# Kernel tuning notes

Hardware: AMD Instinct MI355X
Metric: run time of the kernel (lower is better)

The kernel has to match this reference:

```python
import jax, jax.numpy as jnp
import numpy as np

B, IN, OUT = 384, 512, 384  # B must equal OUT (broadcast in original sigma_3 + diag(sigma_bias))


def setup_inputs() -> dict:
    key = jax.random.key(0)
    k1, k2, k3, k4 = jax.random.split(key, 4)
    mu = jax.random.normal(k1, (B, IN), dtype=jnp.float32)
    sigma = jax.random.uniform(k2, (B, IN, IN), dtype=jnp.float32)
    # nn.Linear weight: normal(0, 0.1); bias filled with 1e-4
    W = 0.1 * jax.random.normal(k3, (OUT, IN), dtype=jnp.float32)
    b = jnp.full((OUT,), 1e-4, dtype=jnp.float32)
    # sigma_weight ~ U(-12, -2.2); sigma_bias = ones * bias(True)
    sigma_weight = jax.random.uniform(k4, (OUT, IN), minval=-12.0, maxval=-2.2, dtype=jnp.float32)
    sigma_bias = jnp.ones((OUT,), dtype=jnp.float32)
    return {"mu": mu, "sigma": sigma, "W": W, "b": b,
            "sigma_weight": sigma_weight, "sigma_bias": sigma_bias}


def reference(mu, sigma, W, b, sigma_weight, sigma_bias):
    sp = jnp.log1p(jnp.exp(sigma_weight))            # softplus(sigma_weight), [OUT, IN]
    mu_f = mu @ W.T + b                              # [B, OUT]
    # sigma_1: diag( sum_i sigma[b,i,i] * sp[o,i] )  (equivalent to the torch
    # diag_embed / batched-matmul / diagonal chain, without the [B,OUT,IN,IN] blowup)
    diag_sigma = jnp.diagonal(sigma, axis1=1, axis2=2)   # [B, IN]
    s1 = jnp.einsum('bi,oi->bo', diag_sigma, sp)         # [B, OUT]
    # sigma_2 = W @ sigma @ W^T, dense part
    s2 = jnp.einsum('oi,bij,pj->bop', W, sigma, W)       # [B, OUT, OUT]
    # sigma_3 = sp @ mu^2 + diag(sigma_bias)  ([B,OUT] + [OUT,OUT], valid since B==OUT)
    s3 = jnp.square(mu) @ sp.T + jnp.diag(sigma_bias)    # [B, OUT]
    eye = jnp.eye(sp.shape[0], dtype=mu.dtype)
    sigma_out = (s1 + s3)[:, :, None] * eye + s2         # [B, OUT, OUT]
    return mu_f, sigma_out
```

## Files before the change

### kernel.cpp

```cpp
#include <hip/hip_runtime.h>
#include <hip/hip_bf16.h>
#include <math.h>

#define Bn   384
#define INn  512
#define OUTn 384

typedef __bf16 bf16x8 __attribute__((ext_vector_type(8)));
typedef __bf16 bf16x4 __attribute__((ext_vector_type(4)));
typedef float  f32x4  __attribute__((ext_vector_type(4)));

__device__ __bf16 g_Wbf[OUTn * INn];
__device__ float  g_sp [OUTn * INn];
__device__ float  g_d  [Bn * OUTn];
__device__ float  g_t  [Bn * INn];
__device__ __bf16 g_U  [(size_t)Bn * OUTn * INn];

__global__ __launch_bounds__(256) void prep_kernel(const float* __restrict__ W,
                                                   const float* __restrict__ sw) {
    int idx = blockIdx.x * 256 + threadIdx.x;
    if (idx < OUTn * INn) {
        g_Wbf[idx] = (__bf16)W[idx];
        float x = sw[idx];
        g_sp[idx] = (x > 20.f) ? x : log1pf(expf(x));
    }
}

__global__ __launch_bounds__(512, 4) void passA_kernel(const float* __restrict__ sigma) {
    __shared__ __bf16 As[64][INn + 8];

    const int it   = blockIdx.x;
    const int b    = blockIdx.y;
    const int tid  = threadIdx.x;
    const int wave = tid >> 6, lane = tid & 63;
    const int quad = lane >> 4, l15 = lane & 15;
    const int i0   = it * 64;

    const float* sigb = sigma + (size_t)b * (INn * INn) + (size_t)i0 * INn;

#pragma unroll
    for (int k = 0; k < 8; ++k) {
        const int r = k * 8 + wave;
        const float* rp = sigb + (size_t)r * INn + lane * 8;
        float4 a0 = *(const float4*)rp;
        float4 a1 = *(const float4*)(rp + 4);
        bf16x8 t;
        t[0]=(__bf16)a0.x; t[1]=(__bf16)a0.y; t[2]=(__bf16)a0.z; t[3]=(__bf16)a0.w;
        t[4]=(__bf16)a1.x; t[5]=(__bf16)a1.y; t[6]=(__bf16)a1.z; t[7]=(__bf16)a1.w;
        *(bf16x8*)&As[r][lane * 8] = t;
        const int ig = i0 + r;
        if ((ig >> 3) == lane) {
            const int c = ig & 7;
            float dv = (c==0)?a0.x:(c==1)?a0.y:(c==2)?a0.z:(c==3)?a0.w
                     :(c==4)?a1.x:(c==5)?a1.y:(c==6)?a1.z:a1.w;
            g_t[b * INn + ig] = dv;
        }
    }
    __syncthreads();

    const int p_base = wave * 48;
    f32x4 acc[4][3];
#pragma unroll
    for (int mi = 0; mi < 4; ++mi)
#pragma unroll
        for (int nf = 0; nf < 3; ++nf) acc[mi][nf] = (f32x4){0.f, 0.f, 0.f, 0.f};

    for (int kc = 0; kc < INn; kc += 32) {
        bf16x8 afr[4];
#pragma unroll
        for (int mi = 0; mi < 4; ++mi)
            afr[mi] = *(const bf16x8*)&As[mi * 16 + l15][kc + quad * 8];
#pragma unroll
        for (int nf = 0; nf < 3; ++nf) {
            const __bf16* bp = g_Wbf + (size_t)(p_base + nf * 16 + l15) * INn + kc + quad * 8;
            bf16x8 bfr = *(const bf16x8*)bp;
#pragma unroll
            for (int mi = 0; mi < 4; ++mi)
                acc[mi][nf] = __builtin_amdgcn_mfma_f32_16x16x32_bf16(afr[mi], bfr, acc[mi][nf], 0, 0, 0);
        }
    }

    __bf16* Ub = g_U + (size_t)b * (OUTn * INn);
#pragma unroll
    for (int mi = 0; mi < 4; ++mi) {
        const int ib = i0 + mi * 16 + quad * 4;
#pragma unroll
        for (int nf = 0; nf < 3; ++nf) {
            const int p = p_base + nf * 16 + l15;
            bf16x4 v;
            v[0] = (__bf16)acc[mi][nf][0];
            v[1] = (__bf16)acc[mi][nf][1];
            v[2] = (__bf16)acc[mi][nf][2];
            v[3] = (__bf16)acc[mi][nf][3];
            *(bf16x4*)(Ub + (size_t)p * INn + ib) = v;
        }
    }
}

__global__ __launch_bounds__(256) void k2_kernel(const float* __restrict__ mu,
                                                 const float* __restrict__ W,
                                                 const float* __restrict__ bias,
                                                 const float* __restrict__ sbias,
                                                 float* __restrict__ out_muf) {
    const int b  = blockIdx.x;
    const int oq = blockIdx.y;
    __shared__ __align__(16) float muL[INn];
    __shared__ __align__(16) float tL[INn];
    const int tid = threadIdx.x;
    for (int i = tid; i < INn; i += 256) {
        float m = mu[b * INn + i];
        muL[i] = m;
        tL[i] = g_t[b * INn + i] + m * m;
    }
    __syncthreads();
    const int wave = tid >> 6, lane = tid & 63;
    const float4* Mr = (const float4*)muL;
    const float4* Tr = (const float4*)tL;
    float4 m0 = Mr[lane * 2], m1 = Mr[lane * 2 + 1];
    float4 t0 = Tr[lane * 2], t1 = Tr[lane * 2 + 1];
#pragma unroll 4
    for (int ow = 0; ow < 24; ++ow) {
        const int o = oq * 96 + wave * 24 + ow;
        const float4* Wr = (const float4*)(W + (size_t)o * INn);
        const float4* Sr = (const float4*)(g_sp + (size_t)o * INn);
        float4 w0 = Wr[lane * 2], w1 = Wr[lane * 2 + 1];
        float4 s0 = Sr[lane * 2], s1 = Sr[lane * 2 + 1];
        float mf = w0.x * m0.x + w0.y * m0.y + w0.z * m0.z + w0.w * m0.w
                 + w1.x * m1.x + w1.y * m1.y + w1.z * m1.z + w1.w * m1.w;
        float dd = s0.x * t0.x + s0.y * t0.y + s0.z * t0.z + s0.w * t0.w
                 + s1.x * t1.x + s1.y * t1.y + s1.z * t1.z + s1.w * t1.w;
#pragma unroll
        for (int off = 32; off; off >>= 1) {
            mf += __shfl_xor(mf, off, 64);
            dd += __shfl_xor(dd, off, 64);
        }
        if (lane == 0) {
            out_muf[b * OUTn + o] = mf + bias[o];
            g_d[b * OUTn + o] = dd + (o == b ? sbias[o] : 0.f);
        }
    }
}

__global__ __launch_bounds__(512, 4) void passB_kernel(float* __restrict__ outS) {
    __shared__ __bf16 Ut[64][INn + 8];

    const int ptile = blockIdx.x;
    const int b     = blockIdx.y;
    const int tid   = threadIdx.x;
    const int wave  = tid >> 6, lane = tid & 63;
    const int quad  = lane >> 4, l15 = lane & 15;
    const int p0    = ptile * 64;

    const __bf16* Ub = g_U + ((size_t)b * OUTn + p0) * INn;
#pragma unroll
    for (int k = 0; k < 8; ++k) {
        const int r = k * 8 + wave;
        *(bf16x8*)&Ut[r][lane * 8] = *(const bf16x8*)(Ub + (size_t)r * INn + lane * 8);
    }
    __syncthreads();

    const int o_base = wave * 48;
    f32x4 acc[3][4];
#pragma unroll
    for (int mi = 0; mi < 3; ++mi)
#pragma unroll
        for (int nf = 0; nf < 4; ++nf) acc[mi][nf] = (f32x4){0.f, 0.f, 0.f, 0.f};

    for (int kc = 0; kc < INn; kc += 32) {
        bf16x8 afr[3];
#pragma unroll
        for (int mi = 0; mi < 3; ++mi) {
            const __bf16* ap = g_Wbf + (size_t)(o_base + mi * 16 + l15) * INn + kc + quad * 8;
            afr[mi] = *(const bf16x8*)ap;
        }
#pragma unroll
        for (int nf = 0; nf < 4; ++nf) {
            bf16x8 bfr = *(const bf16x8*)&Ut[nf * 16 + l15][kc + quad * 8];
#pragma unroll
            for (int mi = 0; mi < 3; ++mi)
                acc[mi][nf] = __builtin_amdgcn_mfma_f32_16x16x32_bf16(afr[mi], bfr, acc[mi][nf], 0, 0, 0);
        }
    }

    float* outb = outS + (size_t)b * (OUTn * OUTn);
#pragma unroll
    for (int mi = 0; mi < 3; ++mi) {
        const int o_r = o_base + mi * 16 + quad * 4;
#pragma unroll
        for (int nf = 0; nf < 4; ++nf) {
            const int p = p0 + nf * 16 + l15;
#pragma unroll
            for (int r = 0; r < 4; ++r) {
                const int o = o_r + r;
                float v = acc[mi][nf][r];
                if (o == p) v += g_d[b * OUTn + o];
                outb[(size_t)o * OUTn + p] = v;
            }
        }
    }
}

extern "C" void kernel_launch(void* const* d_in, const int* in_sizes, int n_in,
                              void* d_out, int out_size, void* d_ws, size_t ws_size,
                              hipStream_t stream) {
    const float* mu    = (const float*)d_in[0];
    const float* sigma = (const float*)d_in[1];
    const float* W     = (const float*)d_in[2];
    const float* bias  = (const float*)d_in[3];
    const float* sw    = (const float*)d_in[4];
    const float* sbias = (const float*)d_in[5];

    float* out     = (float*)d_out;
    float* out_muf = out;
    float* out_sig = out + Bn * OUTn;

    prep_kernel<<<(OUTn * INn + 255) / 256, 256, 0, stream>>>(W, sw);
    passA_kernel<<<dim3(8, Bn), 512, 0, stream>>>(sigma);
    k2_kernel<<<dim3(Bn, 4), 256, 0, stream>>>(mu, W, bias, sbias, out_muf);
    passB_kernel<<<dim3(6, Bn), 512, 0, stream>>>(out_sig);
}
```

Measured before the change: 930.5 us.

## Drop LDS staging in both GEMM passes and retile pass A to 32-row blocks

Pass A no longer stages a 64-row sigma tile in shared memory. Each block of 4 waves now handles 32 rows and reads its fp32 sigma fragments straight from global memory into registers, converting to bf16 on the fly, while each wave covers 96 output columns. The sigma diagonal extraction moves into the K loop. Pass B also drops its LDS tile of U and loads B fragments directly from global memory. The aim is to remove LDS traffic and the barrier and to raise occupancy, relying on L2 cache reuse, at the cost of more redundant global loads across waves.

```diff
diff --git a/kernel.cpp b/kernel.cpp
--- a/kernel.cpp
+++ b/kernel.cpp
@@ -26,66 +26,59 @@
     }
 }
 
-__global__ __launch_bounds__(512, 4) void passA_kernel(const float* __restrict__ sigma) {
-    __shared__ __bf16 As[64][INn + 8];
-
+__global__ __launch_bounds__(256, 3) void passA_kernel(const float* __restrict__ sigma) {
     const int it   = blockIdx.x;
     const int b    = blockIdx.y;
     const int tid  = threadIdx.x;
     const int wave = tid >> 6, lane = tid & 63;
     const int quad = lane >> 4, l15 = lane & 15;
-    const int i0   = it * 64;
-
-    const float* sigb = sigma + (size_t)b * (INn * INn) + (size_t)i0 * INn;
-
-#pragma unroll
-    for (int k = 0; k < 8; ++k) {
-        const int r = k * 8 + wave;
-        const float* rp = sigb + (size_t)r * INn + lane * 8;
-        float4 a0 = *(const float4*)rp;
-        float4 a1 = *(const float4*)(rp + 4);
-        bf16x8 t;
-        t[0]=(__bf16)a0.x; t[1]=(__bf16)a0.y; t[2]=(__bf16)a0.z; t[3]=(__bf16)a0.w;
-        t[4]=(__bf16)a1.x; t[5]=(__bf16)a1.y; t[6]=(__bf16)a1.z; t[7]=(__bf16)a1.w;
-        *(bf16x8*)&As[r][lane * 8] = t;
-        const int ig = i0 + r;
-        if ((ig >> 3) == lane) {
-            const int c = ig & 7;
-            float dv = (c==0)?a0.x:(c==1)?a0.y:(c==2)?a0.z:(c==3)?a0.w
-                     :(c==4)?a1.x:(c==5)?a1.y:(c==6)?a1.z:a1.w;
-            g_t[b * INn + ig] = dv;
-        }
-    }
-    __syncthreads();
-
-    const int p_base = wave * 48;
-    f32x4 acc[4][3];
-#pragma unroll
-    for (int mi = 0; mi < 4; ++mi)
-#pragma unroll
-        for (int nf = 0; nf < 3; ++nf) acc[mi][nf] = (f32x4){0.f, 0.f, 0.f, 0.f};
+    const int i0     = it * 32;
+    const int p_base = wave * 96;
+
+    const float* sigb = sigma + (size_t)b * (INn * INn);
+
+    f32x4 acc[2][6];
+#pragma unroll
+    for (int mi = 0; mi < 2; ++mi)
+#pragma unroll
+        for (int nf = 0; nf < 6; ++nf) acc[mi][nf] = (f32x4){0.f, 0.f, 0.f, 0.f};
 
     for (int kc = 0; kc < INn; kc += 32) {
-        bf16x8 afr[4];
-#pragma unroll
-        for (int mi = 0; mi < 4; ++mi)
-            afr[mi] = *(const bf16x8*)&As[mi * 16 + l15][kc + quad * 8];
-#pragma unroll
-        for (int nf = 0; nf < 3; ++nf) {
+        bf16x8 afr[2];
+#pragma unroll
+        for (int mi = 0; mi < 2; ++mi) {
+            const int row = i0 + mi * 16 + l15;
+            const float* ap = sigb + (size_t)row * INn + kc + quad * 8;
+            float4 a0 = *(const float4*)ap;
+            float4 a1 = *(const float4*)(ap + 4);
+            if (wave == 0) {
+                const int j = row - (kc + quad * 8);
+                if (j >= 0 && j < 8) {
+                    float dv = (j==0)?a0.x:(j==1)?a0.y:(j==2)?a0.z:(j==3)?a0.w
+                             :(j==4)?a1.x:(j==5)?a1.y:(j==6)?a1.z:a1.w;
+                    g_t[b * INn + row] = dv;
+                }
+            }
+            bf16x8 t;
+            t[0]=(__bf16)a0.x; t[1]=(__bf16)a0.y; t[2]=(__bf16)a0.z; t[3]=(__bf16)a0.w;
+            t[4]=(__bf16)a1.x; t[5]=(__bf16)a1.y; t[6]=(__bf16)a1.z; t[7]=(__bf16)a1.w;
+            afr[mi] = t;
+        }
+#pragma unroll
+        for (int nf = 0; nf < 6; ++nf) {
             const __bf16* bp = g_Wbf + (size_t)(p_base + nf * 16 + l15) * INn + kc + quad * 8;
             bf16x8 bfr = *(const bf16x8*)bp;
-#pragma unroll
-            for (int mi = 0; mi < 4; ++mi)
-                acc[mi][nf] = __builtin_amdgcn_mfma_f32_16x16x32_bf16(afr[mi], bfr, acc[mi][nf], 0, 0, 0);
+            acc[0][nf] = __builtin_amdgcn_mfma_f32_16x16x32_bf16(afr[0], bfr, acc[0][nf], 0, 0, 0);
+            acc[1][nf] = __builtin_amdgcn_mfma_f32_16x16x32_bf16(afr[1], bfr, acc[1][nf], 0, 0, 0);
         }
     }
 
     __bf16* Ub = g_U + (size_t)b * (OUTn * INn);
 #pragma unroll
-    for (int mi = 0; mi < 4; ++mi) {
+    for (int mi = 0; mi < 2; ++mi) {
         const int ib = i0 + mi * 16 + quad * 4;
 #pragma unroll
-        for (int nf = 0; nf < 3; ++nf) {
+        for (int nf = 0; nf < 6; ++nf) {
             const int p = p_base + nf * 16 + l15;
             bf16x4 v;
             v[0] = (__bf16)acc[mi][nf][0];
@@ -142,24 +135,16 @@
 }
 
 __global__ __launch_bounds__(512, 4) void passB_kernel(float* __restrict__ outS) {
-    __shared__ __bf16 Ut[64][INn + 8];
-
     const int ptile = blockIdx.x;
     const int b     = blockIdx.y;
     const int tid   = threadIdx.x;
     const int wave  = tid >> 6, lane = tid & 63;
     const int quad  = lane >> 4, l15 = lane & 15;
-    const int p0    = ptile * 64;
+    const int p0     = ptile * 64;
+    const int o_base = wave * 48;
 
     const __bf16* Ub = g_U + ((size_t)b * OUTn + p0) * INn;
-#pragma unroll
-    for (int k = 0; k < 8; ++k) {
-        const int r = k * 8 + wave;
-        *(bf16x8*)&Ut[r][lane * 8] = *(const bf16x8*)(Ub + (size_t)r * INn + lane * 8);
-    }
-    __syncthreads();
-
-    const int o_base = wave * 48;
+
     f32x4 acc[3][4];
 #pragma unroll
     for (int mi = 0; mi < 3; ++mi)
@@ -175,7 +160,8 @@
         }
 #pragma unroll
         for (int nf = 0; nf < 4; ++nf) {
-            bf16x8 bfr = *(const bf16x8*)&Ut[nf * 16 + l15][kc + quad * 8];
+            const __bf16* bp = Ub + (size_t)(nf * 16 + l15) * INn + kc + quad * 8;
+            bf16x8 bfr = *(const bf16x8*)bp;
 #pragma unroll
             for (int mi = 0; mi < 3; ++mi)
                 acc[mi][nf] = __builtin_amdgcn_mfma_f32_16x16x32_bf16(afr[mi], bfr, acc[mi][nf], 0, 0, 0);
@@ -215,7 +201,7 @@
     float* out_sig = out + Bn * OUTn;
 
     prep_kernel<<<(OUTn * INn + 255) / 256, 256, 0, stream>>>(W, sw);
-    passA_kernel<<<dim3(8, Bn), 512, 0, stream>>>(sigma);
+    passA_kernel<<<dim3(16, Bn), 256, 0, stream>>>(sigma);
     k2_kernel<<<dim3(Bn, 4), 256, 0, stream>>>(mu, W, bias, sbias, out_muf);
     passB_kernel<<<dim3(6, Bn), 512, 0, stream>>>(out_sig);
 }
```

Measured after the change: 1.301 ms. 39.8% more time.

## Double-buffer K chunks in passA/passB and transpose W/softplus for k2

Applied to the files above, without the earlier changes.

Both GEMM passes now stage their shared-memory operand in 128-wide K chunks with a double buffer, so global loads of the next chunk overlap MFMA work on the current one. This shrinks LDS per block, which can raise occupancy, at the cost of extra barriers. k2 is rewritten to one thread per output column reading transposed W and softplus arrays built in prep, replacing the wave-reduction scheme. The transposed writes in prep are strided and uncoalesced.

```diff
diff --git a/kernel.cpp b/kernel.cpp
--- a/kernel.cpp
+++ b/kernel.cpp
@@ -11,7 +11,8 @@
 typedef float  f32x4  __attribute__((ext_vector_type(4)));
 
 __device__ __bf16 g_Wbf[OUTn * INn];
-__device__ float  g_sp [OUTn * INn];
+__device__ float  g_Wt [INn * OUTn];
+__device__ float  g_spt[INn * OUTn];
 __device__ float  g_d  [Bn * OUTn];
 __device__ float  g_t  [Bn * INn];
 __device__ __bf16 g_U  [(size_t)Bn * OUTn * INn];
@@ -20,65 +21,89 @@
                                                    const float* __restrict__ sw) {
     int idx = blockIdx.x * 256 + threadIdx.x;
     if (idx < OUTn * INn) {
-        g_Wbf[idx] = (__bf16)W[idx];
+        const int o = idx >> 9, i = idx & 511;
+        float w = W[idx];
+        g_Wbf[idx] = (__bf16)w;
+        g_Wt[i * OUTn + o] = w;
         float x = sw[idx];
-        g_sp[idx] = (x > 20.f) ? x : log1pf(expf(x));
+        g_spt[i * OUTn + o] = (x > 20.f) ? x : log1pf(expf(x));
     }
 }
 
 __global__ __launch_bounds__(512, 4) void passA_kernel(const float* __restrict__ sigma) {
-    __shared__ __bf16 As[64][INn + 8];
+    __shared__ __bf16 As[2][64][136];
 
     const int it   = blockIdx.x;
     const int b    = blockIdx.y;
     const int tid  = threadIdx.x;
     const int wave = tid >> 6, lane = tid & 63;
     const int quad = lane >> 4, l15 = lane & 15;
-    const int i0   = it * 64;
-
-    const float* sigb = sigma + (size_t)b * (INn * INn) + (size_t)i0 * INn;
-
-#pragma unroll
-    for (int k = 0; k < 8; ++k) {
-        const int r = k * 8 + wave;
-        const float* rp = sigb + (size_t)r * INn + lane * 8;
-        float4 a0 = *(const float4*)rp;
-        float4 a1 = *(const float4*)(rp + 4);
-        bf16x8 t;
-        t[0]=(__bf16)a0.x; t[1]=(__bf16)a0.y; t[2]=(__bf16)a0.z; t[3]=(__bf16)a0.w;
-        t[4]=(__bf16)a1.x; t[5]=(__bf16)a1.y; t[6]=(__bf16)a1.z; t[7]=(__bf16)a1.w;
-        *(bf16x8*)&As[r][lane * 8] = t;
-        const int ig = i0 + r;
-        if ((ig >> 3) == lane) {
-            const int c = ig & 7;
-            float dv = (c==0)?a0.x:(c==1)?a0.y:(c==2)?a0.z:(c==3)?a0.w
-                     :(c==4)?a1.x:(c==5)?a1.y:(c==6)?a1.z:a1.w;
+    const int i0     = it * 64;
+    const int p_base = wave * 48;
+    const int srow   = tid >> 3;
+    const int scol   = (tid & 7) * 16;
+
+    const float* sigb   = sigma + (size_t)b * (INn * INn);
+    const float* srcRow = sigb + (size_t)(i0 + srow) * INn + scol;
+
+    float4 r0, r1, r2, r3;
+
+    auto LOAD = [&](int c) {
+        const float4* p = (const float4*)(srcRow + c * 128);
+        r0 = p[0]; r1 = p[1]; r2 = p[2]; r3 = p[3];
+    };
+    auto STORE = [&](int c, int buf) {
+        const int ig   = i0 + srow;
+        const int base = c * 128 + scol;
+        if (ig >= base && ig < base + 16) {
+            const int j = ig - base;
+            float4 v = (j < 4) ? r0 : (j < 8) ? r1 : (j < 12) ? r2 : r3;
+            const int e = j & 3;
+            float dv = (e == 0) ? v.x : (e == 1) ? v.y : (e == 2) ? v.z : v.w;
             g_t[b * INn + ig] = dv;
         }
-    }
+        bf16x8 t0, t1;
+        t0[0]=(__bf16)r0.x; t0[1]=(__bf16)r0.y; t0[2]=(__bf16)r0.z; t0[3]=(__bf16)r0.w;
+        t0[4]=(__bf16)r1.x; t0[5]=(__bf16)r1.y; t0[6]=(__bf16)r1.z; t0[7]=(__bf16)r1.w;
+        t1[0]=(__bf16)r2.x; t1[1]=(__bf16)r2.y; t1[2]=(__bf16)r2.z; t1[3]=(__bf16)r2.w;
+        t1[4]=(__bf16)r3.x; t1[5]=(__bf16)r3.y; t1[6]=(__bf16)r3.z; t1[7]=(__bf16)r3.w;
+        *(bf16x8*)&As[buf][srow][scol]     = t0;
+        *(bf16x8*)&As[buf][srow][scol + 8] = t1;
+    };
+
+    f32x4 acc[4][3];
+#pragma unroll
+    for (int mi = 0; mi < 4; ++mi)
+#pragma unroll
+        for (int nf = 0; nf < 3; ++nf) acc[mi][nf] = (f32x4){0.f, 0.f, 0.f, 0.f};
+
+    auto COMPUTE = [&](int buf, int kc0) {
+#pragma unroll
+        for (int kcl = 0; kcl < 128; kcl += 32) {
+            bf16x8 afr[4];
+#pragma unroll
+            for (int mi = 0; mi < 4; ++mi)
+                afr[mi] = *(const bf16x8*)&As[buf][mi * 16 + l15][kcl + quad * 8];
+#pragma unroll
+            for (int nf = 0; nf < 3; ++nf) {
+                const __bf16* bp = g_Wbf + (size_t)(p_base + nf * 16 + l15) * INn + kc0 + kcl + quad * 8;
+                bf16x8 bfr = *(const bf16x8*)bp;
+#pragma unroll
+                for (int mi = 0; mi < 4; ++mi)
+                    acc[mi][nf] = __builtin_amdgcn_mfma_f32_16x16x32_bf16(afr[mi], bfr, acc[mi][nf], 0, 0, 0);
+            }
+        }
+    };
+
+    LOAD(0); STORE(0, 0); LOAD(1);
     __syncthreads();
-
-    const int p_base = wave * 48;
-    f32x4 acc[4][3];
-#pragma unroll
-    for (int mi = 0; mi < 4; ++mi)
-#pragma unroll
-        for (int nf = 0; nf < 3; ++nf) acc[mi][nf] = (f32x4){0.f, 0.f, 0.f, 0.f};
-
-    for (int kc = 0; kc < INn; kc += 32) {
-        bf16x8 afr[4];
-#pragma unroll
-        for (int mi = 0; mi < 4; ++mi)
-            afr[mi] = *(const bf16x8*)&As[mi * 16 + l15][kc + quad * 8];
-#pragma unroll
-        for (int nf = 0; nf < 3; ++nf) {
-            const __bf16* bp = g_Wbf + (size_t)(p_base + nf * 16 + l15) * INn + kc + quad * 8;
-            bf16x8 bfr = *(const bf16x8*)bp;
-#pragma unroll
-            for (int mi = 0; mi < 4; ++mi)
-                acc[mi][nf] = __builtin_amdgcn_mfma_f32_16x16x32_bf16(afr[mi], bfr, acc[mi][nf], 0, 0, 0);
-        }
-    }
+    COMPUTE(0, 0);
+    __syncthreads(); STORE(1, 1); LOAD(2); __syncthreads();
+    COMPUTE(1, 128);
+    __syncthreads(); STORE(2, 0); LOAD(3); __syncthreads();
+    COMPUTE(0, 256);
+    __syncthreads(); STORE(3, 1); __syncthreads();
+    COMPUTE(1, 384);
 
     __bf16* Ub = g_U + (size_t)b * (OUTn * INn);
 #pragma unroll
@@ -97,90 +122,91 @@
     }
 }
 
-__global__ __launch_bounds__(256) void k2_kernel(const float* __restrict__ mu,
-                                                 const float* __restrict__ W,
+__global__ __launch_bounds__(384) void k2_kernel(const float* __restrict__ mu,
                                                  const float* __restrict__ bias,
                                                  const float* __restrict__ sbias,
                                                  float* __restrict__ out_muf) {
-    const int b  = blockIdx.x;
-    const int oq = blockIdx.y;
+    const int b = blockIdx.x;
+    const int t = threadIdx.x;
     __shared__ __align__(16) float muL[INn];
     __shared__ __align__(16) float tL[INn];
-    const int tid = threadIdx.x;
-    for (int i = tid; i < INn; i += 256) {
+    for (int i = t; i < INn; i += 384) {
         float m = mu[b * INn + i];
         muL[i] = m;
         tL[i] = g_t[b * INn + i] + m * m;
     }
     __syncthreads();
-    const int wave = tid >> 6, lane = tid & 63;
-    const float4* Mr = (const float4*)muL;
-    const float4* Tr = (const float4*)tL;
-    float4 m0 = Mr[lane * 2], m1 = Mr[lane * 2 + 1];
-    float4 t0 = Tr[lane * 2], t1 = Tr[lane * 2 + 1];
-#pragma unroll 4
-    for (int ow = 0; ow < 24; ++ow) {
-        const int o = oq * 96 + wave * 24 + ow;
-        const float4* Wr = (const float4*)(W + (size_t)o * INn);
-        const float4* Sr = (const float4*)(g_sp + (size_t)o * INn);
-        float4 w0 = Wr[lane * 2], w1 = Wr[lane * 2 + 1];
-        float4 s0 = Sr[lane * 2], s1 = Sr[lane * 2 + 1];
-        float mf = w0.x * m0.x + w0.y * m0.y + w0.z * m0.z + w0.w * m0.w
-                 + w1.x * m1.x + w1.y * m1.y + w1.z * m1.z + w1.w * m1.w;
-        float dd = s0.x * t0.x + s0.y * t0.y + s0.z * t0.z + s0.w * t0.w
-                 + s1.x * t1.x + s1.y * t1.y + s1.z * t1.z + s1.w * t1.w;
-#pragma unroll
-        for (int off = 32; off; off >>= 1) {
-            mf += __shfl_xor(mf, off, 64);
-            dd += __shfl_xor(dd, off, 64);
-        }
-        if (lane == 0) {
-            out_muf[b * OUTn + o] = mf + bias[o];
-            g_d[b * OUTn + o] = dd + (o == b ? sbias[o] : 0.f);
-        }
-    }
+    float mf = 0.f, dd = 0.f;
+#pragma unroll 8
+    for (int i = 0; i < INn; ++i) {
+        mf += g_Wt[i * OUTn + t] * muL[i];
+        dd += g_spt[i * OUTn + t] * tL[i];
+    }
+    out_muf[b * OUTn + t] = mf + bias[t];
+    g_d[b * OUTn + t] = dd + (t == b ? sbias[t] : 0.f);
 }
 
 __global__ __launch_bounds__(512, 4) void passB_kernel(float* __restrict__ outS) {
-    __shared__ __bf16 Ut[64][INn + 8];
+    __shared__ __bf16 Ut[2][64][136];
 
     const int ptile = blockIdx.x;
     const int b     = blockIdx.y;
     const int tid   = threadIdx.x;
     const int wave  = tid >> 6, lane = tid & 63;
     const int quad  = lane >> 4, l15 = lane & 15;
-    const int p0    = ptile * 64;
-
-    const __bf16* Ub = g_U + ((size_t)b * OUTn + p0) * INn;
-#pragma unroll
-    for (int k = 0; k < 8; ++k) {
-        const int r = k * 8 + wave;
-        *(bf16x8*)&Ut[r][lane * 8] = *(const bf16x8*)(Ub + (size_t)r * INn + lane * 8);
-    }
+    const int p0     = ptile * 64;
+    const int o_base = wave * 48;
+    const int srow   = tid >> 3;
+    const int scol   = (tid & 7) * 16;
+
+    const __bf16* Ub     = g_U + ((size_t)b * OUTn + p0) * INn;
+    const __bf16* srcRow = Ub + (size_t)srow * INn + scol;
+
+    bf16x8 u0, u1;
+
+    auto LOAD = [&](int c) {
+        const bf16x8* p = (const bf16x8*)(srcRow + c * 128);
+        u0 = p[0]; u1 = p[1];
+    };
+    auto STORE = [&](int buf) {
+        *(bf16x8*)&Ut[buf][srow][scol]     = u0;
+        *(bf16x8*)&Ut[buf][srow][scol + 8] = u1;
+    };
+
+    f32x4 acc[3][4];
+#pragma unroll
+    for (int mi = 0; mi < 3; ++mi)
+#pragma unroll
+        for (int nf = 0; nf < 4; ++nf) acc[mi][nf] = (f32x4){0.f, 0.f, 0.f, 0.f};
+
+    auto COMPUTE = [&](int buf, int kc0) {
+#pragma unroll
+        for (int kcl = 0; kcl < 128; kcl += 32) {
+            bf16x8 afr[3];
+#pragma unroll
+            for (int mi = 0; mi < 3; ++mi) {
+                const __bf16* ap = g_Wbf + (size_t)(o_base + mi * 16 + l15) * INn + kc0 + kcl + quad * 8;
+                afr[mi] = *(const bf16x8*)ap;
+            }
+#pragma unroll
+            for (int nf = 0; nf < 4; ++nf) {
+                bf16x8 bfr = *(const bf16x8*)&Ut[buf][nf * 16 + l15][kcl + quad * 8];
+#pragma unroll
+                for (int mi = 0; mi < 3; ++mi)
+                    acc[mi][nf] = __builtin_amdgcn_mfma_f32_16x16x32_bf16(afr[mi], bfr, acc[mi][nf], 0, 0, 0);
+            }
+        }
+    };
+
+    LOAD(0); STORE(0); LOAD(1);
     __syncthreads();
-
-    const int o_base = wave * 48;
-    f32x4 acc[3][4];
-#pragma unroll
-    for (int mi = 0; mi < 3; ++mi)
-#pragma unroll
-        for (int nf = 0; nf < 4; ++nf) acc[mi][nf] = (f32x4){0.f, 0.f, 0.f, 0.f};
-
-    for (int kc = 0; kc < INn; kc += 32) {
-        bf16x8 afr[3];
-#pragma unroll
-        for (int mi = 0; mi < 3; ++mi) {
-            const __bf16* ap = g_Wbf + (size_t)(o_base + mi * 16 + l15) * INn + kc + quad * 8;
-            afr[mi] = *(const bf16x8*)ap;
-        }
-#pragma unroll
-        for (int nf = 0; nf < 4; ++nf) {
-            bf16x8 bfr = *(const bf16x8*)&Ut[nf * 16 + l15][kc + quad * 8];
-#pragma unroll
-            for (int mi = 0; mi < 3; ++mi)
-                acc[mi][nf] = __builtin_amdgcn_mfma_f32_16x16x32_bf16(afr[mi], bfr, acc[mi][nf], 0, 0, 0);
-        }
-    }
+    COMPUTE(0, 0);
+    __syncthreads(); STORE(1); LOAD(2); __syncthreads();
+    COMPUTE(1, 128);
+    __syncthreads(); STORE(0); LOAD(3); __syncthreads();
+    COMPUTE(0, 256);
+    __syncthreads(); STORE(1); __syncthreads();
+    COMPUTE(1, 384);
 
     float* outb = outS + (size_t)b * (OUTn * OUTn);
 #pragma unroll
@@ -216,6 +242,6 @@
 
     prep_kernel<<<(OUTn * INn + 255) / 256, 256, 0, stream>>>(W, sw);
     passA_kernel<<<dim3(8, Bn), 512, 0, stream>>>(sigma);
-    k2_kernel<<<dim3(Bn, 4), 256, 0, stream>>>(mu, W, bias, sbias, out_muf);
+    k2_kernel<<<Bn, 384, 0, stream>>>(mu, bias, sbias, out_muf);
     passB_kernel<<<dim3(6, Bn), 512, 0, stream>>>(out_sig);
 }
```

Measured after the change: 1.054 ms. 1.13x slower.
